# Optimization experiments

Measured on AMD Instinct MI355X. Metric: run time of the kernel, lower is better.

The kernel has to match this reference:

```python
import jax, jax.numpy as jnp
import numpy as np

ALPHA, BETA, GAMMA = 1.0, 0.01, 0.1
COS_EPS = 1e-8  # torch F.cosine_similarity eps


def setup_inputs() -> dict:
    key = jax.random.key(0)
    k1, k2, k3, k4 = jax.random.split(key, 4)
    B, C = 4096, 1000
    N, D = 8192, 256
    return {
        "pred": jax.random.normal(k1, (B, C), dtype=jnp.float32),
        "target": jax.random.randint(k2, (B,), 0, C, dtype=jnp.int64),
        "adj_matrix": jax.random.uniform(k3, (N, N), dtype=jnp.float32),
        "node_embeddings": jax.random.normal(k4, (N, D), dtype=jnp.float32),
    }


def reference(pred, target, adj_matrix, node_embeddings):
    # L_task: mean cross-entropy over logits
    logp = jax.nn.log_softmax(pred, axis=-1)                      # [B, C]
    l_task = -jnp.mean(jnp.take_along_axis(logp, target[:, None], axis=1))

    # L_sparse: mean |adj|
    l_sparse = jnp.mean(jnp.abs(adj_matrix))

    # L_semantic: cosine similarity via normalize + matmul (avoids NxNxD intermediate)
    norms = jnp.linalg.norm(node_embeddings, axis=1)              # [N]
    dots = node_embeddings @ node_embeddings.T                    # [N, N]
    sim = dots / jnp.maximum(norms[:, None] * norms[None, :], COS_EPS)
    l_semantic = jnp.mean(adj_matrix * (1.0 - sim))

    return ALPHA * l_task + BETA * l_sparse + GAMMA * l_semantic
```

## Files before the change

kernel.cpp:

```cpp
#include <hip/hip_runtime.h>
#include <hip/hip_bf16.h>
#include <stdint.h>
#include <stddef.h>

#define N_NODES 8192
#define DIM     256
#define BATCH   4096
#define CLASSES 1000
#define ALPHA_C 1.0f
#define BETA_C  0.01f
#define GAMMA_C 0.1f

typedef __bf16 bf16_t;
typedef __bf16 bf16x8 __attribute__((ext_vector_type(8)));
typedef float  f32x4  __attribute__((ext_vector_type(4)));
typedef float  f32x16 __attribute__((ext_vector_type(16)));

__device__ __forceinline__ void async16(const void* g, void* l) {
  __builtin_amdgcn_global_load_lds(
      (const __attribute__((address_space(1))) uint32_t*)g,
      (__attribute__((address_space(3))) uint32_t*)l, 16, 0, 0);
}

__global__ __launch_bounds__(256) void prep_kernel(
    const float* __restrict__ emb, bf16_t* __restrict__ U) {
  const int row = blockIdx.x;
  const int t = threadIdx.x;
  const float v = emb[(size_t)row * DIM + t];
  float sq = v * v;
  for (int off = 32; off; off >>= 1) sq += __shfl_down(sq, off);
  __shared__ float red[4];
  if ((t & 63) == 0) red[t >> 6] = sq;
  __syncthreads();
  const float total = red[0] + red[1] + red[2] + red[3];
  U[(size_t)row * DIM + t] = (bf16_t)(v * rsqrtf(total));
}

__global__ __launch_bounds__(256) void ce_kernel(
    const float* __restrict__ pred, const int* __restrict__ target,
    float* __restrict__ out) {
  const int row = blockIdx.x;
  const int t = threadIdx.x;
  const float* p = pred + (size_t)row * CLASSES;

  float v[4];
  for (int k = 0; k < 4; ++k) {
    const int c = t + k * 256;
    v[k] = (c < CLASSES) ? p[c] : -INFINITY;
  }

  float m = fmaxf(fmaxf(v[0], v[1]), fmaxf(v[2], v[3]));
  for (int off = 32; off; off >>= 1) m = fmaxf(m, __shfl_down(m, off));

  __shared__ float red[8];
  const int wave = t >> 6, lane = t & 63;
  if (lane == 0) red[wave] = m;
  __syncthreads();
  if (t == 0) red[4] = fmaxf(fmaxf(red[0], red[1]), fmaxf(red[2], red[3]));
  __syncthreads();
  const float mx = red[4];

  float s = 0.f;
  for (int k = 0; k < 4; ++k) s += __expf(v[k] - mx);
  for (int off = 32; off; off >>= 1) s += __shfl_down(s, off);
  if (lane == 0) red[wave] = s;
  __syncthreads();
  if (t == 0) {
    float ssum = red[0] + red[1] + red[2] + red[3];
    float lse = mx + __logf(ssum);
    float loss = lse - p[target[row]];
    atomicAdd(out, loss * (ALPHA_C / (float)BATCH));
  }
}

#define BT 128

__global__ __launch_bounds__(256, 3) void gram_kernel(
    const float* __restrict__ adj, const bf16_t* __restrict__ U,
    float* __restrict__ out) {
  __shared__ __align__(16) float lds_f[128 * 68];
  __shared__ float red[4];
  bf16_t* As = (bf16_t*)lds_f;
  bf16_t* Bs = ((bf16_t*)lds_f) + 128 * 64;

  const int bi = blockIdx.y, bj = blockIdx.x;
  const int i0 = bi * BT, j0 = bj * BT;
  const int t = threadIdx.x;
  const int w = t >> 6, lane = t & 63;
  const int wr = (w >> 1) * 64, wc = (w & 1) * 64;
  const int m = lane & 31, h = lane >> 5;

  const int srow = lane >> 3;
  const int schunk = (lane & 7) ^ srow;

  f32x16 acc[2][2] = {};

  for (int kc = 0; kc < 4; ++kc) {
    const int ko = kc * 64;
#pragma unroll
    for (int ii = 0; ii < 4; ++ii) {
      const int rbase = w * 32 + ii * 8;
      async16(U + (size_t)(i0 + rbase + srow) * DIM + ko + schunk * 8,
              &As[rbase * 64]);
      async16(U + (size_t)(j0 + rbase + srow) * DIM + ko + schunk * 8,
              &Bs[rbase * 64]);
    }
    __syncthreads();
#pragma unroll
    for (int kk = 0; kk < 64; kk += 16) {
      const int p = (((kk >> 3) + h) ^ (m & 7)) * 8;
      bf16x8 a0 = *(const bf16x8*)&As[(wr + m) * 64 + p];
      bf16x8 a1 = *(const bf16x8*)&As[(wr + 32 + m) * 64 + p];
      bf16x8 b0 = *(const bf16x8*)&Bs[(wc + m) * 64 + p];
      bf16x8 b1 = *(const bf16x8*)&Bs[(wc + 32 + m) * 64 + p];
      acc[0][0] =
          __builtin_amdgcn_mfma_f32_32x32x16_bf16(a0, b0, acc[0][0], 0, 0, 0);
      acc[0][1] =
          __builtin_amdgcn_mfma_f32_32x32x16_bf16(a0, b1, acc[0][1], 0, 0, 0);
      acc[1][0] =
          __builtin_amdgcn_mfma_f32_32x32x16_bf16(a1, b0, acc[1][0], 0, 0, 0);
      acc[1][1] =
          __builtin_amdgcn_mfma_f32_32x32x16_bf16(a1, b1, acc[1][1], 0, 0, 0);
    }
    __syncthreads();
  }

  float local = 0.f;
  const int g4 = t & 15;
  const int i_rel = ((g4 & 8) ? 64 : 0) + (g4 & 7) * 4;

#pragma unroll
  for (int ms = 0; ms < 2; ++ms) {
#pragma unroll
    for (int ns = 0; ns < 2; ++ns) {
      const int c = wc + ns * 32 + m;
#pragma unroll
      for (int rg = 0; rg < 4; ++rg) {
        const int rh = (w >> 1) * 32 + rg * 8 + h * 4;
        f32x4 vv = {acc[ms][ns][rg * 4 + 0], acc[ms][ns][rg * 4 + 1],
                    acc[ms][ns][rg * 4 + 2], acc[ms][ns][rg * 4 + 3]};
        *(f32x4*)&lds_f[c * 68 + rh] = vv;
      }
    }
    __syncthreads();
    const int i_off = ms * 32 + i_rel;
#pragma unroll
    for (int k = 0; k < 8; ++k) {
      const int c = (t >> 4) + k * 16;
      const f32x4 s = *(const f32x4*)&lds_f[c * 68 + g4 * 4];
      const float4 a4 =
          *(const float4*)&adj[(size_t)(j0 + c) * N_NODES + i0 + i_off];
      local +=
          BETA_C * (fabsf(a4.x) + fabsf(a4.y) + fabsf(a4.z) + fabsf(a4.w));
      local += GAMMA_C * (a4.x * (1.f - s.x) + a4.y * (1.f - s.y) +
                          a4.z * (1.f - s.z) + a4.w * (1.f - s.w));
    }
    __syncthreads();
  }

  for (int off = 32; off; off >>= 1) local += __shfl_down(local, off);
  if (lane == 0) red[w] = local;
  __syncthreads();
  if (t == 0) {
    const float inv = 1.f / ((float)N_NODES * (float)N_NODES);
    atomicAdd(out, (red[0] + red[1] + red[2] + red[3]) * inv);
  }
}

extern "C" void kernel_launch(void* const* d_in, const int* in_sizes, int n_in,
                              void* d_out, int out_size, void* d_ws,
                              size_t ws_size, hipStream_t stream) {
  const float* pred   = (const float*)d_in[0];
  const int*   target = (const int*)d_in[1];
  const float* adj    = (const float*)d_in[2];
  const float* emb    = (const float*)d_in[3];
  float* out = (float*)d_out;

  bf16_t* U = (bf16_t*)d_ws;

  hipMemsetAsync(d_out, 0, sizeof(float), stream);
  prep_kernel<<<N_NODES, 256, 0, stream>>>(emb, U);
  ce_kernel<<<BATCH, 256, 0, stream>>>(pred, target, out);
  gram_kernel<<<dim3(N_NODES / BT, N_NODES / BT), 256, 0, stream>>>(adj, U,
                                                                    out);
}
```

Measured before the change: 471.3 us.

## Reassociate semantic loss as adj@U then dot with U, split-K GEMM

Replaces the N×N Gram computation with the reassociation sum(A∘(U Uᵀ)) = sum(U ∘ (A U)), so the kernel computes an N×D product of adj (converted to bf16 on the fly) with a transposed normalized embedding copy V, then dots the result with U. This cuts MFMA work from N²·D on the Gram to the same order but removes the fp32 similarity tile staging through LDS. adj is read row-wise with register prefetch, split across 16 K-slices, and sums of adj and |adj| are accumulated in the same pass. It adds a transposed bf16 copy written with strided stores in prep, and rounds adj to bf16, which adds numerical error to the semantic term.

```diff
diff --git a/kernel.cpp b/kernel.cpp
--- a/kernel.cpp
+++ b/kernel.cpp
@@ -11,6 +11,11 @@
 #define BETA_C  0.01f
 #define GAMMA_C 0.1f
 
+#define KSPLIT  16
+#define KRANGE  (N_NODES / KSPLIT)
+#define NCHUNK  (KRANGE / 64)
+#define BM      64
+
 typedef __bf16 bf16_t;
 typedef __bf16 bf16x8 __attribute__((ext_vector_type(8)));
 typedef float  f32x4  __attribute__((ext_vector_type(4)));
@@ -23,7 +28,8 @@
 }
 
 __global__ __launch_bounds__(256) void prep_kernel(
-    const float* __restrict__ emb, bf16_t* __restrict__ U) {
+    const float* __restrict__ emb, bf16_t* __restrict__ U,
+    bf16_t* __restrict__ V) {
   const int row = blockIdx.x;
   const int t = threadIdx.x;
   const float v = emb[(size_t)row * DIM + t];
@@ -33,7 +39,9 @@
   if ((t & 63) == 0) red[t >> 6] = sq;
   __syncthreads();
   const float total = red[0] + red[1] + red[2] + red[3];
-  U[(size_t)row * DIM + t] = (bf16_t)(v * rsqrtf(total));
+  const bf16_t u = (bf16_t)(v * rsqrtf(total));
+  U[(size_t)row * DIM + t] = u;
+  V[(size_t)t * N_NODES + row] = u;
 }
 
 __global__ __launch_bounds__(256) void ce_kernel(
@@ -73,46 +81,84 @@
   }
 }
 
-#define BT 128
-
-__global__ __launch_bounds__(256, 3) void gram_kernel(
+__global__ __launch_bounds__(256) void gemm_kernel(
     const float* __restrict__ adj, const bf16_t* __restrict__ U,
-    float* __restrict__ out) {
-  __shared__ __align__(16) float lds_f[128 * 68];
-  __shared__ float red[4];
-  bf16_t* As = (bf16_t*)lds_f;
-  bf16_t* Bs = ((bf16_t*)lds_f) + 128 * 64;
-
-  const int bi = blockIdx.y, bj = blockIdx.x;
-  const int i0 = bi * BT, j0 = bj * BT;
+    const bf16_t* __restrict__ V, float* __restrict__ out) {
+  __shared__ __align__(16) bf16_t As[BM * 64];
+  __shared__ __align__(16) bf16_t Bs[DIM * 64];
+
+  const int i0 = blockIdx.x * BM;
+  const int kbase = blockIdx.y * KRANGE;
   const int t = threadIdx.x;
   const int w = t >> 6, lane = t & 63;
-  const int wr = (w >> 1) * 64, wc = (w & 1) * 64;
   const int m = lane & 31, h = lane >> 5;
 
+  const int ar = t >> 3;
+  const int ac = t & 7;
   const int srow = lane >> 3;
-  const int schunk = (lane & 7) ^ srow;
+  const int sch = (lane & 7) ^ srow;
 
   f32x16 acc[2][2] = {};
-
-  for (int kc = 0; kc < 4; ++kc) {
-    const int ko = kc * 64;
-#pragma unroll
-    for (int ii = 0; ii < 4; ++ii) {
-      const int rbase = w * 32 + ii * 8;
-      async16(U + (size_t)(i0 + rbase + srow) * DIM + ko + schunk * 8,
-              &As[rbase * 64]);
-      async16(U + (size_t)(j0 + rbase + srow) * DIM + ko + schunk * 8,
-              &Bs[rbase * 64]);
+  float sa = 0.f, sabs = 0.f;
+
+  float4 pf[4];
+  {
+    const float* a0p = adj + (size_t)(i0 + ar) * N_NODES + kbase + ac * 8;
+    const float* a1p = adj + (size_t)(i0 + ar + 32) * N_NODES + kbase + ac * 8;
+    pf[0] = *(const float4*)a0p;
+    pf[1] = *(const float4*)(a0p + 4);
+    pf[2] = *(const float4*)a1p;
+    pf[3] = *(const float4*)(a1p + 4);
+  }
+
+  for (int kc = 0; kc < NCHUNK; ++kc) {
+    const int k0 = kbase + kc * 64;
+
+    {
+      bf16x8 c0, c1;
+      c0[0] = (bf16_t)pf[0].x; c0[1] = (bf16_t)pf[0].y;
+      c0[2] = (bf16_t)pf[0].z; c0[3] = (bf16_t)pf[0].w;
+      c0[4] = (bf16_t)pf[1].x; c0[5] = (bf16_t)pf[1].y;
+      c0[6] = (bf16_t)pf[1].z; c0[7] = (bf16_t)pf[1].w;
+      c1[0] = (bf16_t)pf[2].x; c1[1] = (bf16_t)pf[2].y;
+      c1[2] = (bf16_t)pf[2].z; c1[3] = (bf16_t)pf[2].w;
+      c1[4] = (bf16_t)pf[3].x; c1[5] = (bf16_t)pf[3].y;
+      c1[6] = (bf16_t)pf[3].z; c1[7] = (bf16_t)pf[3].w;
+#pragma unroll
+      for (int q = 0; q < 4; ++q) {
+        sa += pf[q].x + pf[q].y + pf[q].z + pf[q].w;
+        sabs += fabsf(pf[q].x) + fabsf(pf[q].y) +
+                fabsf(pf[q].z) + fabsf(pf[q].w);
+      }
+      const int p = (ac ^ (ar & 7)) * 8;
+      *(bf16x8*)&As[ar * 64 + p] = c0;
+      *(bf16x8*)&As[(ar + 32) * 64 + p] = c1;
+    }
+#pragma unroll
+    for (int s = 0; s < 8; ++s) {
+      const int dbase = w * 64 + s * 8;
+      async16(V + (size_t)(dbase + srow) * N_NODES + k0 + sch * 8,
+              &Bs[dbase * 64]);
     }
     __syncthreads();
-#pragma unroll
-    for (int kk = 0; kk < 64; kk += 16) {
-      const int p = (((kk >> 3) + h) ^ (m & 7)) * 8;
-      bf16x8 a0 = *(const bf16x8*)&As[(wr + m) * 64 + p];
-      bf16x8 a1 = *(const bf16x8*)&As[(wr + 32 + m) * 64 + p];
-      bf16x8 b0 = *(const bf16x8*)&Bs[(wc + m) * 64 + p];
-      bf16x8 b1 = *(const bf16x8*)&Bs[(wc + 32 + m) * 64 + p];
+
+    if (kc + 1 < NCHUNK) {
+      const int kn = k0 + 64;
+      const float* a0p = adj + (size_t)(i0 + ar) * N_NODES + kn + ac * 8;
+      const float* a1p = adj + (size_t)(i0 + ar + 32) * N_NODES + kn + ac * 8;
+      pf[0] = *(const float4*)a0p;
+      pf[1] = *(const float4*)(a0p + 4);
+      pf[2] = *(const float4*)a1p;
+      pf[3] = *(const float4*)(a1p + 4);
+    }
+
+#pragma unroll
+    for (int kk = 0; kk < 4; ++kk) {
+      const int p = ((kk * 2 + h) ^ (m & 7)) * 8;
+      bf16x8 a0 = *(const bf16x8*)&As[m * 64 + p];
+      bf16x8 a1 = *(const bf16x8*)&As[(m + 32) * 64 + p];
+      bf16x8 b0 = *(const bf16x8*)&Bs[(w * 64 + m) * 64 + p];
+      bf16x8 b1 = *(const bf16x8*)&Bs[(w * 64 + 32 + m) * 64 + p];
       acc[0][0] =
           __builtin_amdgcn_mfma_f32_32x32x16_bf16(a0, b0, acc[0][0], 0, 0, 0);
       acc[0][1] =
@@ -125,45 +171,30 @@
     __syncthreads();
   }
 
-  float local = 0.f;
-  const int g4 = t & 15;
-  const int i_rel = ((g4 & 8) ? 64 : 0) + (g4 & 7) * 4;
-
-#pragma unroll
-  for (int ms = 0; ms < 2; ++ms) {
-#pragma unroll
-    for (int ns = 0; ns < 2; ++ns) {
-      const int c = wc + ns * 32 + m;
-#pragma unroll
-      for (int rg = 0; rg < 4; ++rg) {
-        const int rh = (w >> 1) * 32 + rg * 8 + h * 4;
-        f32x4 vv = {acc[ms][ns][rg * 4 + 0], acc[ms][ns][rg * 4 + 1],
-                    acc[ms][ns][rg * 4 + 2], acc[ms][ns][rg * 4 + 3]};
-        *(f32x4*)&lds_f[c * 68 + rh] = vv;
+  float simdot = 0.f;
+#pragma unroll
+  for (int mi = 0; mi < 2; ++mi) {
+#pragma unroll
+    for (int nd = 0; nd < 2; ++nd) {
+      const int ib = i0 + mi * 32 + 4 * h;
+      const int d = w * 64 + nd * 32 + m;
+      const bf16_t* up = U + (size_t)ib * DIM + d;
+#pragma unroll
+      for (int rg = 0; rg < 16; ++rg) {
+        const int row = (rg & 3) + 8 * (rg >> 2);
+        simdot += (float)up[(size_t)row * DIM] * acc[mi][nd][rg];
       }
     }
-    __syncthreads();
-    const int i_off = ms * 32 + i_rel;
-#pragma unroll
-    for (int k = 0; k < 8; ++k) {
-      const int c = (t >> 4) + k * 16;
-      const f32x4 s = *(const f32x4*)&lds_f[c * 68 + g4 * 4];
-      const float4 a4 =
-          *(const float4*)&adj[(size_t)(j0 + c) * N_NODES + i0 + i_off];
-      local +=
-          BETA_C * (fabsf(a4.x) + fabsf(a4.y) + fabsf(a4.z) + fabsf(a4.w));
-      local += GAMMA_C * (a4.x * (1.f - s.x) + a4.y * (1.f - s.y) +
-                          a4.z * (1.f - s.z) + a4.w * (1.f - s.w));
-    }
-    __syncthreads();
-  }
-
+  }
+
+  float local = BETA_C * sabs + GAMMA_C * (sa - simdot);
   for (int off = 32; off; off >>= 1) local += __shfl_down(local, off);
-  if (lane == 0) red[w] = local;
+  float* redf = (float*)As;
+  if (lane == 0) redf[w] = local;
   __syncthreads();
   if (t == 0) {
     const float inv = 1.f / ((float)N_NODES * (float)N_NODES);
-    atomicAdd(out, (red[0] + red[1] + red[2] + red[3]) * inv);
+    atomicAdd(out, (redf[0] + redf[1] + redf[2] + redf[3]) * inv);
   }
 }
 
@@ -177,10 +208,10 @@
   float* out = (float*)d_out;
 
   bf16_t* U = (bf16_t*)d_ws;
+  bf16_t* V = (bf16_t*)((char*)d_ws + (size_t)N_NODES * DIM * 2);
 
   hipMemsetAsync(d_out, 0, sizeof(float), stream);
-  prep_kernel<<<N_NODES, 256, 0, stream>>>(emb, U);
+  prep_kernel<<<N_NODES, 256, 0, stream>>>(emb, U, V);
   ce_kernel<<<BATCH, 256, 0, stream>>>(pred, target, out);
-  gram_kernel<<<dim3(N_NODES / BT, N_NODES / BT), 256, 0, stream>>>(adj, U,
-                                                                    out);
-}
+  gemm_kernel<<<dim3(N_NODES / BM, KSPLIT), 256, 0, stream>>>(adj, U, V, out);
+}
```

Result: slower. 489.5 us (+3.9%).
